# Kernel tuning notes

Hardware: AMD Instinct MI355X
Metric: run time of the kernel (lower is better)

## Reference

```python
import jax, jax.numpy as jnp
import numpy as np

MARGIN = 0.5

def setup_inputs() -> dict:
    key = jax.random.key(0)
    k1, k2 = jax.random.split(key)
    logits = jax.random.normal(k1, (4096, 128), dtype=jnp.float32)
    labels = jax.random.randint(k2, (4096, 128), 0, 2, dtype=jnp.int32)
    return {"logits": logits, "labels": labels}

def reference(logits, labels):
    # pos/neg masks per row
    pos = labels > 0            # [B, D]
    neg = labels == 0           # [B, D]
    # pairwise relu(margin - (pos_score - neg_score)) over all (i, j) doc pairs
    diff = logits[:, :, None] - logits[:, None, :]          # [B, D, D]
    pl = jax.nn.relu(MARGIN - diff)                         # [B, D, D]
    pair_mask = (pos[:, :, None] & neg[:, None, :]).astype(logits.dtype)  # [B, D, D]
    row_sum = jnp.sum(pl * pair_mask, axis=(1, 2))          # [B]
    counts = jnp.sum(pair_mask, axis=(1, 2))                # [B]
    valid = counts > 0
    row_mean = jnp.where(valid, row_sum / jnp.maximum(counts, 1.0), 0.0)
    n_valid = jnp.sum(valid.astype(logits.dtype))
    # mean over rows that have at least one (pos, neg) pair; 0.0 if none
    return jnp.where(n_valid > 0, jnp.sum(row_mean) / jnp.maximum(n_valid, 1.0), 0.0)
```

## Files before the change

kernel.cpp:

```cpp
#include <hip/hip_runtime.h>

#define MARGIN 0.5f
#define NROWS 4096
#define D 128
#define ROWS_PER_BLOCK 4
#define NBLOCKS (NROWS / ROWS_PER_BLOCK)

__global__ __launch_bounds__(256) void mrl_row_kernel(
    const float* __restrict__ logits,
    const int*   __restrict__ labels,
    float* __restrict__ partial_sum,
    float* __restrict__ partial_val)
{
    const int wave = threadIdx.x >> 6;
    const int lane = threadIdx.x & 63;
    const int row  = blockIdx.x * ROWS_PER_BLOCK + wave;

    __shared__ float s_neg[ROWS_PER_BLOCK][132];
    __shared__ float s_pos[ROWS_PER_BLOCK][132];
    __shared__ float sb_sum[ROWS_PER_BLOCK];
    __shared__ float sb_val[ROWS_PER_BLOCK];

    const float* lrow   = logits + (size_t)row * D;
    const int*   labrow = labels + (size_t)row * D;

    const int i0 = lane * 2;
    float2 lv = *reinterpret_cast<const float2*>(lrow + i0);
    int2   bv = *reinterpret_cast<const int2*>(labrow + i0);

    const bool n0 = (bv.x == 0), n1 = (bv.y == 0);
    const bool p0 = (bv.x > 0),  p1 = (bv.y > 0);

    const unsigned long long mn0 = __ballot(n0);
    const unsigned long long mn1 = __ballot(n1);
    const unsigned long long mp0 = __ballot(p0);
    const unsigned long long mp1 = __ballot(p1);
    const unsigned long long below = (1ull << lane) - 1ull;

    const int nneg = __popcll(mn0) + __popcll(mn1);
    const int npos = __popcll(mp0) + __popcll(mp1);

    if (n0) s_neg[wave][__popcll(mn0 & below)]                 = lv.x;
    if (n1) s_neg[wave][__popcll(mn0) + __popcll(mn1 & below)] = lv.y;
    if (p0) s_pos[wave][__popcll(mp0 & below)]                 = MARGIN - lv.x;
    if (p1) s_pos[wave][__popcll(mp0) + __popcll(mp1 & below)] = MARGIN - lv.y;

    if (lane < 4) s_neg[wave][nneg + lane] = -3.0e38f;

    __syncthreads();

    const int nneg4 = (nneg + 3) >> 2;
    const float4* vp = reinterpret_cast<const float4*>(s_neg[wave]);

    float acc = 0.f;
    for (int p = lane; p < npos; p += 64) {
        const float c = s_pos[wave][p];
        float a = 0.f;
#pragma unroll 2
        for (int q = 0; q < nneg4; ++q) {
            float4 v = vp[q];
            a += fmaxf(v.x + c, 0.f);
            a += fmaxf(v.y + c, 0.f);
            a += fmaxf(v.z + c, 0.f);
            a += fmaxf(v.w + c, 0.f);
        }
        acc += a;
    }

    for (int off = 32; off > 0; off >>= 1)
        acc += __shfl_xor(acc, off);

    if (lane == 0) {
        const int cnt = npos * nneg;
        sb_sum[wave] = (cnt > 0) ? acc / (float)cnt : 0.f;
        sb_val[wave] = (cnt > 0) ? 1.f : 0.f;
    }
    __syncthreads();
    if (threadIdx.x == 0) {
        partial_sum[blockIdx.x] = sb_sum[0] + sb_sum[1] + sb_sum[2] + sb_sum[3];
        partial_val[blockIdx.x] = sb_val[0] + sb_val[1] + sb_val[2] + sb_val[3];
    }
}

__global__ __launch_bounds__(256) void mrl_reduce_kernel(
    const float* __restrict__ partial_sum,
    const float* __restrict__ partial_val,
    float* __restrict__ out)
{
    float s = 0.f, v = 0.f;
    for (int i = threadIdx.x; i < NBLOCKS; i += 256) {
        s += partial_sum[i];
        v += partial_val[i];
    }
    for (int off = 32; off > 0; off >>= 1) {
        s += __shfl_xor(s, off);
        v += __shfl_xor(v, off);
    }
    __shared__ float ss[4], sv[4];
    const int wave = threadIdx.x >> 6;
    const int lane = threadIdx.x & 63;
    if (lane == 0) { ss[wave] = s; sv[wave] = v; }
    __syncthreads();
    if (threadIdx.x == 0) {
        float S = ss[0] + ss[1] + ss[2] + ss[3];
        float V = sv[0] + sv[1] + sv[2] + sv[3];
        out[0] = (V > 0.f) ? S / V : 0.f;
    }
}

extern "C" void kernel_launch(void* const* d_in, const int* in_sizes, int n_in,
                              void* d_out, int out_size, void* d_ws, size_t ws_size,
                              hipStream_t stream) {
    const float* logits = (const float*)d_in[0];
    const int*   labels = (const int*)d_in[1];
    float* out = (float*)d_out;
    float* ws  = (float*)d_ws;

    mrl_row_kernel<<<NBLOCKS, 256, 0, stream>>>(logits, labels, ws, ws + NBLOCKS);
    mrl_reduce_kernel<<<1, 256, 0, stream>>>(ws, ws + NBLOCKS, out);
}
```

Baseline: 11.90 us.

## Fuse final reduction into row kernel via last-block atomic ticket

Merges the separate reduce kernel into the row kernel. Each block publishes its partial sums with atomic stores and increments a global ticket counter, and the block that observes the final ticket value does the global reduction. This removes one kernel launch and its inter-kernel gap. It also swaps the block-wide barrier after the shared-memory scatter for a wave barrier, since each wave touches only its own row slice. The ticket relies on uninitialised workspace wrapping modulo NBLOCKS, which assumes the counter starts at a multiple of NBLOCKS.

```diff
diff --git a/kernel.cpp b/kernel.cpp
--- a/kernel.cpp
+++ b/kernel.cpp
@@ -3,23 +3,26 @@
 #define MARGIN 0.5f
 #define NROWS 4096
 #define D 128
-#define ROWS_PER_BLOCK 4
-#define NBLOCKS (NROWS / ROWS_PER_BLOCK)
+#define WAVES_PER_BLOCK 4
+#define NBLOCKS (NROWS / WAVES_PER_BLOCK)
 
-__global__ __launch_bounds__(256) void mrl_row_kernel(
+__global__ __launch_bounds__(256) void mrl_fused_kernel(
     const float* __restrict__ logits,
     const int*   __restrict__ labels,
-    float* __restrict__ partial_sum,
-    float* __restrict__ partial_val)
+    float*        __restrict__ psum,
+    float*        __restrict__ pval,
+    unsigned int* __restrict__ ticket,
+    float*        __restrict__ out)
 {
     const int wave = threadIdx.x >> 6;
     const int lane = threadIdx.x & 63;
-    const int row  = blockIdx.x * ROWS_PER_BLOCK + wave;
+    const int row  = blockIdx.x * WAVES_PER_BLOCK + wave;
 
-    __shared__ float s_neg[ROWS_PER_BLOCK][132];
-    __shared__ float s_pos[ROWS_PER_BLOCK][132];
-    __shared__ float sb_sum[ROWS_PER_BLOCK];
-    __shared__ float sb_val[ROWS_PER_BLOCK];
+    __shared__ float s_neg[WAVES_PER_BLOCK][132];
+    __shared__ float s_pos[WAVES_PER_BLOCK][132];
+    __shared__ float sb_sum[WAVES_PER_BLOCK];
+    __shared__ float sb_val[WAVES_PER_BLOCK];
+    __shared__ int   s_last;
 
     const float* lrow   = logits + (size_t)row * D;
     const int*   labrow = labels + (size_t)row * D;
@@ -47,7 +50,7 @@
 
     if (lane < 4) s_neg[wave][nneg + lane] = -3.0e38f;
 
-    __syncthreads();
+    __builtin_amdgcn_wave_barrier();
 
     const int nneg4 = (nneg + 3) >> 2;
     const float4* vp = reinterpret_cast<const float4*>(s_neg[wave]);
@@ -76,34 +79,34 @@
         sb_val[wave] = (cnt > 0) ? 1.f : 0.f;
     }
     __syncthreads();
+
     if (threadIdx.x == 0) {
-        partial_sum[blockIdx.x] = sb_sum[0] + sb_sum[1] + sb_sum[2] + sb_sum[3];
-        partial_val[blockIdx.x] = sb_val[0] + sb_val[1] + sb_val[2] + sb_val[3];
+        const float S = sb_sum[0] + sb_sum[1] + sb_sum[2] + sb_sum[3];
+        const float V = sb_val[0] + sb_val[1] + sb_val[2] + sb_val[3];
+        __hip_atomic_store(&psum[blockIdx.x], S, __ATOMIC_RELAXED, __HIP_MEMORY_SCOPE_AGENT);
+        __hip_atomic_store(&pval[blockIdx.x], V, __ATOMIC_RELAXED, __HIP_MEMORY_SCOPE_AGENT);
+        const unsigned int old =
+            __hip_atomic_fetch_add(ticket, 1u, __ATOMIC_ACQ_REL, __HIP_MEMORY_SCOPE_AGENT);
+        s_last = (((old + 1u) & (NBLOCKS - 1u)) == 0u) ? 1 : 0;
     }
-}
+    __syncthreads();
+    if (!s_last) return;
 
-__global__ __launch_bounds__(256) void mrl_reduce_kernel(
-    const float* __restrict__ partial_sum,
-    const float* __restrict__ partial_val,
-    float* __restrict__ out)
-{
     float s = 0.f, v = 0.f;
     for (int i = threadIdx.x; i < NBLOCKS; i += 256) {
-        s += partial_sum[i];
-        v += partial_val[i];
+        s += __hip_atomic_load(&psum[i], __ATOMIC_RELAXED, __HIP_MEMORY_SCOPE_AGENT);
+        v += __hip_atomic_load(&pval[i], __ATOMIC_RELAXED, __HIP_MEMORY_SCOPE_AGENT);
     }
     for (int off = 32; off > 0; off >>= 1) {
         s += __shfl_xor(s, off);
         v += __shfl_xor(v, off);
     }
-    __shared__ float ss[4], sv[4];
-    const int wave = threadIdx.x >> 6;
-    const int lane = threadIdx.x & 63;
-    if (lane == 0) { ss[wave] = s; sv[wave] = v; }
+    __syncthreads();
+    if (lane == 0) { sb_sum[wave] = s; sb_val[wave] = v; }
     __syncthreads();
     if (threadIdx.x == 0) {
-        float S = ss[0] + ss[1] + ss[2] + ss[3];
-        float V = sv[0] + sv[1] + sv[2] + sv[3];
+        const float S = sb_sum[0] + sb_sum[1] + sb_sum[2] + sb_sum[3];
+        const float V = sb_val[0] + sb_val[1] + sb_val[2] + sb_val[3];
         out[0] = (V > 0.f) ? S / V : 0.f;
     }
 }
@@ -115,7 +118,9 @@
     const int*   labels = (const int*)d_in[1];
     float* out = (float*)d_out;
     float* ws  = (float*)d_ws;
+    float* psum = ws;
+    float* pval = ws + NBLOCKS;
+    unsigned int* ticket = (unsigned int*)(ws + 2 * NBLOCKS);
 
-    mrl_row_kernel<<<NBLOCKS, 256, 0, stream>>>(logits, labels, ws, ws + NBLOCKS);
-    mrl_reduce_kernel<<<1, 256, 0, stream>>>(ws, ws + NBLOCKS, out);
+    mrl_fused_kernel<<<NBLOCKS, 256, 0, stream>>>(logits, labels, psum, pval, ticket, out);
 }
```

Result: slower. 27.95 us (+134.8%).

## Use 16-wave blocks, wave barrier for row staging, packed float2 partials

Applied to the files above, without the earlier changes.

Each block now handles 16 rows with 1024 threads, giving 256 blocks instead of 1024. The block-wide barrier before the pairwise loop becomes a wave-level barrier, since each wave only reads its own shared-memory row. Partial sums and valid counts are packed into one float2 and reduced with shuffles, so the final reduce kernel does a single load per thread. This cuts block count, barrier cost and partial traffic, but the larger blocks may lower scheduling flexibility and occupancy on a GPU with 256 CUs.

```diff
diff --git a/kernel.cpp b/kernel.cpp
--- a/kernel.cpp
+++ b/kernel.cpp
@@ -3,23 +3,21 @@
 #define MARGIN 0.5f
 #define NROWS 4096
 #define D 128
-#define ROWS_PER_BLOCK 4
-#define NBLOCKS (NROWS / ROWS_PER_BLOCK)
+#define BLK_WAVES 16
+#define NBLK (NROWS / BLK_WAVES)
 
-__global__ __launch_bounds__(256) void mrl_row_kernel(
+__global__ __launch_bounds__(1024) void mrl_row_kernel(
     const float* __restrict__ logits,
     const int*   __restrict__ labels,
-    float* __restrict__ partial_sum,
-    float* __restrict__ partial_val)
+    float2* __restrict__ partial)
 {
     const int wave = threadIdx.x >> 6;
     const int lane = threadIdx.x & 63;
-    const int row  = blockIdx.x * ROWS_PER_BLOCK + wave;
+    const int row  = blockIdx.x * BLK_WAVES + wave;
 
-    __shared__ float s_neg[ROWS_PER_BLOCK][132];
-    __shared__ float s_pos[ROWS_PER_BLOCK][132];
-    __shared__ float sb_sum[ROWS_PER_BLOCK];
-    __shared__ float sb_val[ROWS_PER_BLOCK];
+    __shared__ float  s_neg[BLK_WAVES][132];
+    __shared__ float  s_pos[BLK_WAVES][132];
+    __shared__ float2 sw[BLK_WAVES];
 
     const float* lrow   = logits + (size_t)row * D;
     const int*   labrow = labels + (size_t)row * D;
@@ -47,7 +45,7 @@
 
     if (lane < 4) s_neg[wave][nneg + lane] = -3.0e38f;
 
-    __syncthreads();
+    __builtin_amdgcn_wave_barrier();
 
     const int nneg4 = (nneg + 3) >> 2;
     const float4* vp = reinterpret_cast<const float4*>(s_neg[wave]);
@@ -72,38 +70,38 @@
 
     if (lane == 0) {
         const int cnt = npos * nneg;
-        sb_sum[wave] = (cnt > 0) ? acc / (float)cnt : 0.f;
-        sb_val[wave] = (cnt > 0) ? 1.f : 0.f;
+        sw[wave] = (cnt > 0) ? make_float2(acc / (float)cnt, 1.f)
+                             : make_float2(0.f, 0.f);
     }
     __syncthreads();
-    if (threadIdx.x == 0) {
-        partial_sum[blockIdx.x] = sb_sum[0] + sb_sum[1] + sb_sum[2] + sb_sum[3];
-        partial_val[blockIdx.x] = sb_val[0] + sb_val[1] + sb_val[2] + sb_val[3];
+
+    if (wave == 0) {
+        float2 t = (lane < BLK_WAVES) ? sw[lane] : make_float2(0.f, 0.f);
+        for (int off = 8; off > 0; off >>= 1) {
+            t.x += __shfl_xor(t.x, off);
+            t.y += __shfl_xor(t.y, off);
+        }
+        if (lane == 0) partial[blockIdx.x] = t;
     }
 }
 
 __global__ __launch_bounds__(256) void mrl_reduce_kernel(
-    const float* __restrict__ partial_sum,
-    const float* __restrict__ partial_val,
+    const float2* __restrict__ partial,
     float* __restrict__ out)
 {
-    float s = 0.f, v = 0.f;
-    for (int i = threadIdx.x; i < NBLOCKS; i += 256) {
-        s += partial_sum[i];
-        v += partial_val[i];
+    float2 t = partial[threadIdx.x];
+    for (int off = 32; off > 0; off >>= 1) {
+        t.x += __shfl_xor(t.x, off);
+        t.y += __shfl_xor(t.y, off);
     }
-    for (int off = 32; off > 0; off >>= 1) {
-        s += __shfl_xor(s, off);
-        v += __shfl_xor(v, off);
-    }
-    __shared__ float ss[4], sv[4];
+    __shared__ float2 sw[4];
     const int wave = threadIdx.x >> 6;
     const int lane = threadIdx.x & 63;
-    if (lane == 0) { ss[wave] = s; sv[wave] = v; }
+    if (lane == 0) sw[wave] = t;
     __syncthreads();
     if (threadIdx.x == 0) {
-        float S = ss[0] + ss[1] + ss[2] + ss[3];
-        float V = sv[0] + sv[1] + sv[2] + sv[3];
+        const float S = sw[0].x + sw[1].x + sw[2].x + sw[3].x;
+        const float V = sw[0].y + sw[1].y + sw[2].y + sw[3].y;
         out[0] = (V > 0.f) ? S / V : 0.f;
     }
 }
@@ -114,8 +112,8 @@
     const float* logits = (const float*)d_in[0];
     const int*   labels = (const int*)d_in[1];
     float* out = (float*)d_out;
-    float* ws  = (float*)d_ws;
+    float2* partial = (float2*)d_ws;
 
-    mrl_row_kernel<<<NBLOCKS, 256, 0, stream>>>(logits, labels, ws, ws + NBLOCKS);
-    mrl_reduce_kernel<<<1, 256, 0, stream>>>(ws, ws + NBLOCKS, out);
+    mrl_row_kernel<<<NBLK, 1024, 0, stream>>>(logits, labels, partial);
+    mrl_reduce_kernel<<<1, 256, 0, stream>>>(partial, out);
 }
```

After: 12.18 us. 1.02x slower.
